# Optimization experiments

Hardware: AMD Instinct MI355X
Metric: run time of the kernel (lower is better)

The kernel has to match this reference:

```python
import jax, jax.numpy as jnp
import numpy as np
import math

NX = 240
XL = 6.0
A_ORB = 2
V0 = -20.0
S_INT = 0.5
ITERMAX = 500
FFAC = 0.4


def _wfho(n, x):
    # harmonic-oscillator eigenfunction (numpy, setup only)
    nfac = math.factorial(n)
    norm = (2.0 ** n * nfac) ** (-0.5) / math.pi ** 0.25
    if n == 0:
        Hn = np.ones_like(x)
    elif n == 1:
        Hn = 2.0 * x
    else:
        hm2 = np.ones_like(x)
        hm1 = 2.0 * x
        for m in range(2, n + 1):
            hmx = 2.0 * x * hm1 - 2.0 * (m - 1) * hm2
            hm2, hm1 = hm1, hmx
        Hn = hmx
    return norm * np.exp(-x ** 2 / 2.0) * Hn


def setup_inputs() -> dict:
    delx = 2.0 * XL / NX
    xx = delx * (np.arange(NX) - NX / 2.0)
    delp = 2.0 * math.pi / (2.0 * XL)
    pp = delp * (np.arange(NX) - NX / 2.0)
    # cder2[i,j] = sum_k exp(1j*(xj-xi)*pp_k) * pp_k^2 ; only real part is used
    D = xx[None, :] - xx[:, None]                      # [Nx, Nx], xj - xi
    cder2_re = np.cos(D[:, :, None] * pp[None, None, :]) @ (pp ** 2)
    der2 = -cder2_re * delx * delp / (2.0 * math.pi)
    kin = -der2 / 2.0
    pfac = 1.0 / abs(kin.max())
    U_HO = xx ** 2 / 2.0
    x1, x2 = np.meshgrid(xx, xx, indexing='ij')
    Vint = V0 * (2.0 * math.pi) ** (-0.5) / S_INT * np.exp(-(x1 - x2) ** 2 / (2.0 * S_INT ** 2))
    wfy0 = np.stack([_wfho(n, xx) for n in range(A_ORB)], axis=1)  # [Nx, Nmax]
    return {
        'wfy0': jnp.asarray(wfy0, jnp.float32),
        'kin_mat': jnp.asarray(kin, jnp.float32),
        'Vint': jnp.asarray(Vint, jnp.float32),
        'U_HO': jnp.asarray(U_HO, jnp.float32),
        'delx': jnp.float32(delx),
        'pfac': jnp.float32(pfac),
        'itermax': ITERMAX,
    }


def reference(wfy0, kin_mat, Vint, U_HO, delx, pfac, itermax):
    Nmax = wfy0.shape[1]
    delx = jnp.asarray(delx, jnp.float32).reshape(())
    pfac = jnp.asarray(pfac, jnp.float32).reshape(())

    def step(wfy, _):
        # densities from current orbitals
        hf_den = jnp.sum(wfy ** 2, axis=1)            # [Nx]
        hf_den_mat = wfy @ wfy.T                      # [Nx, Nx]
        Udir = delx * (Vint @ hf_den)
        Umf_mat = -delx * Vint * hf_den_mat
        Umf_mat = Umf_mat + jnp.diag(Udir + U_HO)     # add to diagonal
        H = kin_mat + Umf_mat

        updated = []
        spe = []
        ekin = jnp.float32(0.0)
        epot = jnp.float32(0.0)
        for ieig in range(Nmax):                      # Nmax=2, unrolled
            wf0 = wfy[:, ieig]
            wff = H @ wf0
            spe.append((wf0 @ wff) * delx)
            wfb = wf0 - wff * pfac
            norm = jnp.sum(wfb ** 2) * delx
            wff = wfb / jnp.sqrt(norm)
            for jeig in range(ieig):                  # Gram-Schmidt vs already-updated orbitals
                wff = wff - updated[jeig] * (updated[jeig] @ wff) * delx
            norm = jnp.sum(wff ** 2) * delx
            wff = wff / norm                          # faithful: divide by norm (not sqrt)
            new = FFAC * wff + (1.0 - FFAC) * wf0
            updated.append(new)
            ekin = ekin + (new @ (kin_mat @ new)) * delx
            epot = epot + (new @ (Umf_mat @ new)) * delx
        wfy_new = jnp.stack(updated, axis=1)

        esum0hf = spe[0]
        for s_ in spe[1:]:
            esum0hf = esum0hf + s_
        eho = jnp.sum(hf_den * U_HO) * delx / 2.0
        enerhfp = (esum0hf + ekin) / 2.0 + eho
        epot0hf = epot - 2.0 * eho
        enerhf = esum0hf - epot0hf / 2.0
        out = jnp.stack([enerhf, enerhfp, ekin, eho, epot0hf, esum0hf])
        return wfy_new, out

    _, outs = jax.lax.scan(step, wfy0, None, length=int(itermax))
    return outs[-1]  # (enerhf, enerhfp, ekin0hf, eho, epot0hf, esum0hf)
```

## Files before the change

kernel.cpp:

```cpp
#include <hip/hip_runtime.h>


#define NXX  240
#define NPAD 256
#define NTH  512
#define JCH  60
#define NBLK 15
#define NQW  16

template <int CTRL, int N>
__device__ __forceinline__ void dppStepN(float (&v)[N]) {
#pragma unroll
  for (int k = 0; k < N; ++k) {
    int s = __builtin_amdgcn_update_dpp(0, __float_as_int(v[k]), CTRL, 0xF, 0xF, false);
    v[k] += __int_as_float(s);
  }
}
template <int N>
__device__ __forceinline__ void waveSumDppN(float (&v)[N]) {
  dppStepN<0xB1>(v);
  dppStepN<0x4E>(v);
  dppStepN<0x141>(v);
  dppStepN<0x140>(v);
  dppStepN<0x142>(v);
  dppStepN<0x143>(v);
#pragma unroll
  for (int k = 0; k < N; ++k)
    v[k] = __int_as_float(__builtin_amdgcn_readlane(__float_as_int(v[k]), 63));
}

struct __align__(16) Smem {
  float cK[512];
  float cV[512];
  float uho[NPAD];
  float wfb[2][2][NPAD];
  float p00[NPAD];
  float p01[NPAD];
  float p11[NPAD];
  float part[4][6][NPAD];
};

__global__ void __launch_bounds__(NTH, 2)
hf_kernel(const float* __restrict__ wfy0,
          const float* __restrict__ kin,
          const float* __restrict__ vnt,
          const float* __restrict__ uho_g,
          const float* __restrict__ delx_p,
          const float* __restrict__ pfac_p,
          const int*   __restrict__ iter_p,
          float* __restrict__ out)
{
  __shared__ Smem sm;
  const int t  = (int)threadIdx.x;
  const int wv = t >> 6;
  const int l  = t & 63;
  const int i0 = 4 * l;
  const bool isK = (wv < 4);
  const int g  = isK ? wv : wv - 4;
  const int jg = g * JCH;
  const float delx = delx_p[0];
  const float pfac = pfac_p[0];
  const int itermax = iter_p[0];

  for (int a = t; a < 512; a += NTH) {
    int d = a - 256;
    float vk = 0.f, vv = 0.f;
    if (d >= 0 && d < NXX)      { vk = kin[(size_t)d * NXX]; vv = vnt[(size_t)d * NXX]; }
    else if (d < 0 && -d < NXX) { vk = kin[-d];              vv = vnt[-d]; }
    sm.cK[a] = vk; sm.cV[a] = vv;
  }
  if (t < NPAD) {
    float u  = (t < NXX) ? uho_g[t]        : 0.f;
    float a0 = (t < NXX) ? wfy0[2 * t]     : 0.f;
    float a1 = (t < NXX) ? wfy0[2 * t + 1] : 0.f;
    sm.uho[t] = u;
    sm.wfb[0][0][t] = a0; sm.wfb[0][1][t] = a1;
    sm.wfb[1][0][t] = 0.f; sm.wfb[1][1][t] = 0.f;
    sm.p00[t] = a0 * a0; sm.p01[t] = a0 * a1; sm.p11[t] = a1 * a1;
  }
  __syncthreads();

  const int qb = l - 15 * g + 49;
  const float* tab = isK ? sm.cK : sm.cV;
  float4 cw[NQW];
#pragma unroll
  for (int m = 0; m < NQW; ++m)
    cw[m] = *(const float4*)&tab[4 * (qb + m)];

  int cur = 0;
  for (int it = 0; it < itermax; ++it) {
    const bool last = (it == itermax - 1);
    const float* wf0 = sm.wfb[cur][0];
    const float* wf1 = sm.wfb[cur][1];
    float* nw0 = sm.wfb[cur ^ 1][0];
    float* nw1 = sm.wfb[cur ^ 1][1];

    if (isK) {
      float aK0[4] = {0,0,0,0}, aK1[4] = {0,0,0,0};
#pragma unroll
      for (int b = 0; b < NBLK; ++b) {
        const int j0 = jg + 4 * b;
        const float4 x0 = *(const float4*)&wf0[j0];
        const float4 x1 = *(const float4*)&wf1[j0];
        const float4 kh = cw[15 - b], kl = cw[14 - b];
        const float ck[8] = {kl.x, kl.y, kl.z, kl.w, kh.x, kh.y, kh.z, kh.w};
        const float xs0[4] = {x0.x, x0.y, x0.z, x0.w};
        const float xs1[4] = {x1.x, x1.y, x1.z, x1.w};
#pragma unroll
        for (int s = 0; s < 4; ++s) {
#pragma unroll
          for (int r = 0; r < 4; ++r) {
            const int c = 4 + r - s;
            aK0[r] = fmaf(xs0[s], ck[c], aK0[r]);
            aK1[r] = fmaf(xs1[s], ck[c], aK1[r]);
          }
        }
      }
      *(float4*)&sm.part[g][0][i0] = make_float4(aK0[0], aK0[1], aK0[2], aK0[3]);
      *(float4*)&sm.part[g][1][i0] = make_float4(aK1[0], aK1[1], aK1[2], aK1[3]);
    } else {
      float aV0[4] = {0,0,0,0}, aV1[4] = {0,0,0,0}, aV2[4] = {0,0,0,0};
#pragma unroll
      for (int b = 0; b < NBLK; ++b) {
        const int j0 = jg + 4 * b;
        const float4 y0 = *(const float4*)&sm.p00[j0];
        const float4 y1 = *(const float4*)&sm.p01[j0];
        const float4 y2 = *(const float4*)&sm.p11[j0];
        const float4 vh = cw[15 - b], vl = cw[14 - b];
        const float cv[8] = {vl.x, vl.y, vl.z, vl.w, vh.x, vh.y, vh.z, vh.w};
        const float ys0[4] = {y0.x, y0.y, y0.z, y0.w};
        const float ys1[4] = {y1.x, y1.y, y1.z, y1.w};
        const float ys2[4] = {y2.x, y2.y, y2.z, y2.w};
#pragma unroll
        for (int s = 0; s < 4; ++s) {
#pragma unroll
          for (int r = 0; r < 4; ++r) {
            const int c = 4 + r - s;
            aV0[r] = fmaf(ys0[s], cv[c], aV0[r]);
            aV1[r] = fmaf(ys1[s], cv[c], aV1[r]);
            aV2[r] = fmaf(ys2[s], cv[c], aV2[r]);
          }
        }
      }
      *(float4*)&sm.part[g][2][i0] = make_float4(aV0[0], aV0[1], aV0[2], aV0[3]);
      *(float4*)&sm.part[g][3][i0] = make_float4(aV1[0], aV1[1], aV1[2], aV1[3]);
      *(float4*)&sm.part[g][4][i0] = make_float4(aV2[0], aV2[1], aV2[2], aV2[3]);
    }
    __syncthreads();

    float w0[4], w1[4], Ut[4], wff0[4], wff1[4], new0[4], new1[4];
    float spe0 = 0.f, spe1 = 0.f, eho = 0.f;

    if (wv == 0) {
      const bool valid = (l < 60);
      float k0[4]  = {0,0,0,0}, k1[4]  = {0,0,0,0};
      float v00[4] = {0,0,0,0}, v01[4] = {0,0,0,0}, v11[4] = {0,0,0,0};
#pragma unroll
      for (int gg = 0; gg < 4; ++gg) {
        const float4 A0 = *(const float4*)&sm.part[gg][0][i0];
        const float4 A1 = *(const float4*)&sm.part[gg][1][i0];
        const float4 A2 = *(const float4*)&sm.part[gg][2][i0];
        const float4 A3 = *(const float4*)&sm.part[gg][3][i0];
        const float4 A4 = *(const float4*)&sm.part[gg][4][i0];
        k0[0]  += A0.x; k0[1]  += A0.y; k0[2]  += A0.z; k0[3]  += A0.w;
        k1[0]  += A1.x; k1[1]  += A1.y; k1[2]  += A1.z; k1[3]  += A1.w;
        v00[0] += A2.x; v00[1] += A2.y; v00[2] += A2.z; v00[3] += A2.w;
        v01[0] += A3.x; v01[1] += A3.y; v01[2] += A3.z; v01[3] += A3.w;
        v11[0] += A4.x; v11[1] += A4.y; v11[2] += A4.z; v11[3] += A4.w;
      }
      const float4 w0q = *(const float4*)&wf0[i0];
      const float4 w1q = *(const float4*)&wf1[i0];
      const float4 uq  = *(const float4*)&sm.uho[i0];
      w0[0] = w0q.x; w0[1] = w0q.y; w0[2] = w0q.z; w0[3] = w0q.w;
      w1[0] = w1q.x; w1[1] = w1q.y; w1[2] = w1q.z; w1[3] = w1q.w;
      const float uh[4] = {uq.x, uq.y, uq.z, uq.w};

      float wb0[4], wb1[4];
      float red[6] = {0, 0, 0, 0, 0, 0};
#pragma unroll
      for (int r = 0; r < 4; ++r) {
        Ut[r]   = delx * (v00[r] + v11[r]) + uh[r];
        wff0[r] = k0[r] - delx * (w0[r] * v00[r] + w1[r] * v01[r]) + Ut[r] * w0[r];
        wff1[r] = k1[r] - delx * (w0[r] * v01[r] + w1[r] * v11[r]) + Ut[r] * w1[r];
        wb0[r]  = w0[r] - pfac * wff0[r];
        wb1[r]  = w1[r] - pfac * wff1[r];
        if (!valid) { wb0[r] = 0.f; wb1[r] = 0.f; }
        red[0] += wb0[r] * wb0[r];
        red[1] += wb1[r] * wb1[r];
        red[2] += wb0[r] * wb1[r];
        red[3] += w0[r]  * wb1[r];
        red[4] += wb0[r] * w0[r];
        red[5] += w0[r]  * w0[r];
      }
      waveSumDppN<6>(red);
      const float rdelx = 1.f / delx;
      const float inv0 = 1.f / sqrtf(red[0] * delx);
      const float inv1 = 1.f / sqrtf(red[1] * delx);
      const float dB = delx * inv1 * (0.4f * red[2] * inv0 + 0.6f * red[3]);
      const float e0 = 0.16f * rdelx + 0.48f * red[4] * inv0 + 0.36f * red[5];
      const float sB = rdelx - dB * dB * (2.f * rdelx - e0);
      const float invB = 1.f / (sB * delx);
#pragma unroll
      for (int r = 0; r < 4; ++r) {
        const float wfA  = wb0[r] * inv0;
        const float wfBp = wb1[r] * inv1;
        new0[r] = 0.4f * wfA + 0.6f * w0[r];
        const float wfB2 = wfBp - new0[r] * dB;
        new1[r] = 0.4f * wfB2 * invB + 0.6f * w1[r];
      }
      *(float4*)&nw0[i0] = make_float4(new0[0], new0[1], new0[2], new0[3]);
      *(float4*)&nw1[i0] = make_float4(new1[0], new1[1], new1[2], new1[3]);
      *(float4*)&sm.p00[i0] =
          make_float4(new0[0]*new0[0], new0[1]*new0[1], new0[2]*new0[2], new0[3]*new0[3]);
      *(float4*)&sm.p01[i0] =
          make_float4(new0[0]*new1[0], new0[1]*new1[1], new0[2]*new1[2], new0[3]*new1[3]);
      *(float4*)&sm.p11[i0] =
          make_float4(new1[0]*new1[0], new1[1]*new1[1], new1[2]*new1[2], new1[3]*new1[3]);

      if (last) {
        float er[3] = {0, 0, 0};
#pragma unroll
        for (int r = 0; r < 4; ++r) {
          er[0] += w0[r] * wff0[r];
          er[1] += w1[r] * wff1[r];
          er[2] += (w0[r] * w0[r] + w1[r] * w1[r]) * uh[r];
        }
        waveSumDppN<3>(er);
        spe0 = er[0] * delx; spe1 = er[1] * delx; eho = er[2] * delx * 0.5f;
      }
    }
    __syncthreads();

    if (last) {
      if (isK) {
        float bA0[4] = {0,0,0,0}, bA1[4] = {0,0,0,0};
#pragma unroll
        for (int b = 0; b < NBLK; ++b) {
          const int j0 = jg + 4 * b;
          const float4 n0q = *(const float4*)&nw0[j0];
          const float4 n1q = *(const float4*)&nw1[j0];
          const float4 kh = cw[15 - b], kl = cw[14 - b];
          const float ck[8] = {kl.x, kl.y, kl.z, kl.w, kh.x, kh.y, kh.z, kh.w};
          const float xn0[4] = {n0q.x, n0q.y, n0q.z, n0q.w};
          const float xn1[4] = {n1q.x, n1q.y, n1q.z, n1q.w};
#pragma unroll
          for (int s = 0; s < 4; ++s) {
#pragma unroll
            for (int r = 0; r < 4; ++r) {
              const int c = 4 + r - s;
              bA0[r] = fmaf(xn0[s], ck[c], bA0[r]);
              bA1[r] = fmaf(xn1[s], ck[c], bA1[r]);
            }
          }
        }
        *(float4*)&sm.part[g][0][i0] = make_float4(bA0[0], bA0[1], bA0[2], bA0[3]);
        *(float4*)&sm.part[g][1][i0] = make_float4(bA1[0], bA1[1], bA1[2], bA1[3]);
      } else {
        float bV[4][4] = {};
#pragma unroll
        for (int b = 0; b < NBLK; ++b) {
          const int j0 = jg + 4 * b;
          const float4 o0q = *(const float4*)&wf0[j0];
          const float4 o1q = *(const float4*)&wf1[j0];
          const float4 n0q = *(const float4*)&nw0[j0];
          const float4 n1q = *(const float4*)&nw1[j0];
          const float4 vh = cw[15 - b], vl = cw[14 - b];
          const float cv[8] = {vl.x, vl.y, vl.z, vl.w, vh.x, vh.y, vh.z, vh.w};
          const float xo0[4] = {o0q.x, o0q.y, o0q.z, o0q.w};
          const float xo1[4] = {o1q.x, o1q.y, o1q.z, o1q.w};
          const float xn0[4] = {n0q.x, n0q.y, n0q.z, n0q.w};
          const float xn1[4] = {n1q.x, n1q.y, n1q.z, n1q.w};
#pragma unroll
          for (int s = 0; s < 4; ++s) {
            const float pr00 = xo0[s] * xn0[s];
            const float pr10 = xo1[s] * xn0[s];
            const float pr01 = xo0[s] * xn1[s];
            const float pr11 = xo1[s] * xn1[s];
#pragma unroll
            for (int r = 0; r < 4; ++r) {
              const int c = 4 + r - s;
              bV[0][r] = fmaf(pr00, cv[c], bV[0][r]);
              bV[1][r] = fmaf(pr10, cv[c], bV[1][r]);
              bV[2][r] = fmaf(pr01, cv[c], bV[2][r]);
              bV[3][r] = fmaf(pr11, cv[c], bV[3][r]);
            }
          }
        }
#pragma unroll
        for (int c2 = 0; c2 < 4; ++c2)
          *(float4*)&sm.part[g][2 + c2][i0] =
              make_float4(bV[c2][0], bV[c2][1], bV[c2][2], bV[c2][3]);
      }
      __syncthreads();

      if (wv == 0) {
        float rd[6][4] = {};
#pragma unroll
        for (int gg = 0; gg < 4; ++gg) {
#pragma unroll
          for (int c = 0; c < 6; ++c) {
            const float4 A = *(const float4*)&sm.part[gg][c][i0];
            rd[c][0] += A.x; rd[c][1] += A.y; rd[c][2] += A.z; rd[c][3] += A.w;
          }
        }
        float er[2] = {0, 0};
#pragma unroll
        for (int r = 0; r < 4; ++r) {
          const float um0 = -delx * (w0[r] * rd[2][r] + w1[r] * rd[3][r]) + Ut[r] * new0[r];
          const float um1 = -delx * (w0[r] * rd[4][r] + w1[r] * rd[5][r]) + Ut[r] * new1[r];
          er[0] += new0[r] * rd[0][r] + new1[r] * rd[1][r];
          er[1] += new0[r] * um0 + new1[r] * um1;
        }
        waveSumDppN<2>(er);
        const float ekin = er[0] * delx, epot = er[1] * delx;
        if (l == 0) {
          const float esum    = spe0 + spe1;
          const float enerhfp = 0.5f * (esum + ekin) + eho;
          const float epot0hf = epot - 2.f * eho;
          const float enerhf  = esum - 0.5f * epot0hf;
          out[0] = enerhf; out[1] = enerhfp; out[2] = ekin;
          out[3] = eho;    out[4] = epot0hf; out[5] = esum;
        }
      }
    }
    cur ^= 1;
  }
}

extern "C" void kernel_launch(void* const* d_in, const int* in_sizes, int n_in,
                              void* d_out, int out_size, void* d_ws, size_t ws_size,
                              hipStream_t stream) {
  const float* wfy0 = (const float*)d_in[0];
  const float* kin  = (const float*)d_in[1];
  const float* vnt  = (const float*)d_in[2];
  const float* uho  = (const float*)d_in[3];
  const float* delx = (const float*)d_in[4];
  const float* pfac = (const float*)d_in[5];
  const int*   itm  = (const int*)d_in[6];
  hipLaunchKernelGGL(hf_kernel, dim3(1), dim3(NTH), 0, stream,
                     wfy0, kin, vnt, uho, delx, pfac, itm, (float*)d_out);
}
```

Before: 1.282 ms.

## Use packed fp16 dot2 for Vint convolution and rebalance column chunks

The Vint (direct/exchange potential) convolution now stores the Toeplitz coefficients and the density products as packed fp16 pairs and accumulates with v_dot2_f32_f16, which halves the instruction count and LDS traffic for the V waves. Column chunks change from four equal 60-wide chunks to 64/64/64/48, which suits the packed layout. The V coefficients are now held per lane in a 66-entry register array. The cost is fp16 rounding of the interaction matrix and the densities, which may affect accuracy over 500 iterations, plus higher register pressure.

```diff
diff --git a/kernel.cpp b/kernel.cpp
--- a/kernel.cpp
+++ b/kernel.cpp
@@ -4,9 +4,24 @@
 #define NXX  240
 #define NPAD 256
 #define NTH  512
-#define JCH  60
-#define NBLK 15
-#define NQW  16
+
+typedef _Float16 h2 __attribute__((ext_vector_type(2)));
+
+__device__ __forceinline__ h2 bch2(unsigned u) { union { unsigned u; h2 h; } c; c.u = u; return c.h; }
+__device__ __forceinline__ unsigned bcu(h2 h)  { union { unsigned u; h2 h; } c; c.h = h; return c.u; }
+__device__ __forceinline__ unsigned pkh(float a, float b) {
+  h2 p; p.x = (_Float16)a; p.y = (_Float16)b; return bcu(p);
+}
+
+__device__ __forceinline__ float fdot2(h2 a, h2 b, float c) {
+#if __has_builtin(__builtin_amdgcn_fdot2)
+  return __builtin_amdgcn_fdot2(a, b, c, false);
+#else
+  float d;
+  asm("v_dot2_f32_f16 %0, %1, %2, %3" : "=v"(d) : "v"(a), "v"(b), "v"(c));
+  return d;
+#endif
+}
 
 template <int CTRL, int N>
 __device__ __forceinline__ void dppStepN(float (&v)[N]) {
@@ -31,14 +46,90 @@
 
 struct __align__(16) Smem {
   float cK[512];
-  float cV[512];
+  unsigned pkV[512];
   float uho[NPAD];
   float wfb[2][2][NPAD];
-  float p00[NPAD];
-  float p01[NPAD];
-  float p11[NPAD];
+  unsigned xpk[3][NPAD/2];
+  unsigned xprk[4][NPAD/2];
   float part[4][6][NPAD];
 };
+
+template <int NB>
+__device__ __forceinline__ void kinConv(const float* x0p, const float* x1p, int jg,
+                                        const float4* cw, float (&a0)[4], float (&a1)[4]) {
+#pragma unroll
+  for (int b = 0; b < NB; ++b) {
+    const int j0 = jg + 4 * b;
+    const float4 x0 = *(const float4*)&x0p[j0];
+    const float4 x1 = *(const float4*)&x1p[j0];
+    const float4 kh = cw[16 - b], kl = cw[15 - b];
+    const float ck[8] = {kl.x, kl.y, kl.z, kl.w, kh.x, kh.y, kh.z, kh.w};
+    const float xs0[4] = {x0.x, x0.y, x0.z, x0.w};
+    const float xs1[4] = {x1.x, x1.y, x1.z, x1.w};
+#pragma unroll
+    for (int s = 0; s < 4; ++s)
+#pragma unroll
+      for (int r = 0; r < 4; ++r) {
+        const int c = 4 + r - s;
+        a0[r] = fmaf(xs0[s], ck[c], a0[r]);
+        a1[r] = fmaf(xs1[s], ck[c], a1[r]);
+      }
+  }
+}
+
+template <int NSB>
+__device__ __forceinline__ void vConv3(const unsigned* q0, const unsigned* q1,
+                                       const unsigned* q2, int jg,
+                                       const unsigned* pkw, float (&A)[3][4]) {
+#pragma unroll
+  for (int sb = 0; sb < NSB; ++sb) {
+    const int base = jg / 2 + 4 * sb;
+    const uint4 X0 = *(const uint4*)&q0[base];
+    const uint4 X1 = *(const uint4*)&q1[base];
+    const uint4 X2 = *(const uint4*)&q2[base];
+    const unsigned xs0[4] = {X0.x, X0.y, X0.z, X0.w};
+    const unsigned xs1[4] = {X1.x, X1.y, X1.z, X1.w};
+    const unsigned xs2[4] = {X2.x, X2.y, X2.z, X2.w};
+#pragma unroll
+    for (int p = 0; p < 4; ++p)
+#pragma unroll
+      for (int r = 0; r < 4; ++r) {
+        const int tt = r - 2 * p - 8 * sb + (NSB * 8 - 2);
+        const h2 c = bch2(pkw[tt]);
+        A[0][r] = fdot2(c, bch2(xs0[p]), A[0][r]);
+        A[1][r] = fdot2(c, bch2(xs1[p]), A[1][r]);
+        A[2][r] = fdot2(c, bch2(xs2[p]), A[2][r]);
+      }
+  }
+}
+
+template <int NSB>
+__device__ __forceinline__ void vConv4(const unsigned (*q)[NPAD / 2], int jg,
+                                       const unsigned* pkw, float (&A)[4][4]) {
+#pragma unroll
+  for (int sb = 0; sb < NSB; ++sb) {
+    const int base = jg / 2 + 4 * sb;
+    const uint4 X0 = *(const uint4*)&q[0][base];
+    const uint4 X1 = *(const uint4*)&q[1][base];
+    const uint4 X2 = *(const uint4*)&q[2][base];
+    const uint4 X3 = *(const uint4*)&q[3][base];
+    const unsigned xs0[4] = {X0.x, X0.y, X0.z, X0.w};
+    const unsigned xs1[4] = {X1.x, X1.y, X1.z, X1.w};
+    const unsigned xs2[4] = {X2.x, X2.y, X2.z, X2.w};
+    const unsigned xs3[4] = {X3.x, X3.y, X3.z, X3.w};
+#pragma unroll
+    for (int p = 0; p < 4; ++p)
+#pragma unroll
+      for (int r = 0; r < 4; ++r) {
+        const int tt = r - 2 * p - 8 * sb + (NSB * 8 - 2);
+        const h2 c = bch2(pkw[tt]);
+        A[0][r] = fdot2(c, bch2(xs0[p]), A[0][r]);
+        A[1][r] = fdot2(c, bch2(xs1[p]), A[1][r]);
+        A[2][r] = fdot2(c, bch2(xs2[p]), A[2][r]);
+        A[3][r] = fdot2(c, bch2(xs3[p]), A[3][r]);
+      }
+  }
+}
 
 __global__ void __launch_bounds__(NTH, 2)
 hf_kernel(const float* __restrict__ wfy0,
@@ -57,17 +148,25 @@
   const int i0 = 4 * l;
   const bool isK = (wv < 4);
   const int g  = isK ? wv : wv - 4;
-  const int jg = g * JCH;
+  const int jg = 64 * g;
+  const int len = (g < 3) ? 64 : 48;
   const float delx = delx_p[0];
   const float pfac = pfac_p[0];
   const int itermax = iter_p[0];
 
   for (int a = t; a < 512; a += NTH) {
     int d = a - 256;
-    float vk = 0.f, vv = 0.f;
-    if (d >= 0 && d < NXX)      { vk = kin[(size_t)d * NXX]; vv = vnt[(size_t)d * NXX]; }
-    else if (d < 0 && -d < NXX) { vk = kin[-d];              vv = vnt[-d]; }
-    sm.cK[a] = vk; sm.cV[a] = vv;
+    float vk = 0.f;
+    if (d >= 0 && d < NXX)      vk = kin[(size_t)d * NXX];
+    else if (d < 0 && -d < NXX) vk = kin[-d];
+    sm.cK[a] = vk;
+    float vh = 0.f, vl = 0.f;
+    if (d >= 0 && d < NXX)      vh = vnt[(size_t)d * NXX];
+    else if (d < 0 && -d < NXX) vh = vnt[-d];
+    int d2 = d - 1;
+    if (d2 >= 0 && d2 < NXX)      vl = vnt[(size_t)d2 * NXX];
+    else if (d2 < 0 && -d2 < NXX) vl = vnt[-d2];
+    sm.pkV[a] = pkh(vh, vl);
   }
   if (t < NPAD) {
     float u  = (t < NXX) ? uho_g[t]        : 0.f;
@@ -76,16 +175,31 @@
     sm.uho[t] = u;
     sm.wfb[0][0][t] = a0; sm.wfb[0][1][t] = a1;
     sm.wfb[1][0][t] = 0.f; sm.wfb[1][1][t] = 0.f;
-    sm.p00[t] = a0 * a0; sm.p01[t] = a0 * a1; sm.p11[t] = a1 * a1;
+  }
+  if (t < NPAD / 2) {
+    int j0 = 2 * t, j1 = 2 * t + 1;
+    float w00 = (j0 < NXX) ? wfy0[2 * j0]     : 0.f;
+    float w01 = (j0 < NXX) ? wfy0[2 * j0 + 1] : 0.f;
+    float w10 = (j1 < NXX) ? wfy0[2 * j1]     : 0.f;
+    float w11 = (j1 < NXX) ? wfy0[2 * j1 + 1] : 0.f;
+    sm.xpk[0][t] = pkh(w00 * w00, w10 * w10);
+    sm.xpk[1][t] = pkh(w00 * w01, w10 * w11);
+    sm.xpk[2][t] = pkh(w01 * w01, w11 * w11);
   }
   __syncthreads();
 
-  const int qb = l - 15 * g + 49;
-  const float* tab = isK ? sm.cK : sm.cV;
-  float4 cw[NQW];
-#pragma unroll
-  for (int m = 0; m < NQW; ++m)
-    cw[m] = *(const float4*)&tab[4 * (qb + m)];
+  float4 cw[17];
+  if (isK) {
+    const int qbase = l - 16 * g + 48;
+#pragma unroll
+    for (int m = 0; m < 17; ++m) cw[m] = *(const float4*)&sm.cK[4 * (qbase + m)];
+  }
+  unsigned pkw[66];
+  if (!isK) {
+    const int Abase = i0 - jg - (len - 2) + 256;
+#pragma unroll
+    for (int m = 0; m < 66; ++m) pkw[m] = sm.pkV[Abase + m];
+  }
 
   int cur = 0;
   for (int it = 0; it < itermax; ++it) {
@@ -96,55 +210,19 @@
     float* nw1 = sm.wfb[cur ^ 1][1];
 
     if (isK) {
-      float aK0[4] = {0,0,0,0}, aK1[4] = {0,0,0,0};
-#pragma unroll
-      for (int b = 0; b < NBLK; ++b) {
-        const int j0 = jg + 4 * b;
-        const float4 x0 = *(const float4*)&wf0[j0];
-        const float4 x1 = *(const float4*)&wf1[j0];
-        const float4 kh = cw[15 - b], kl = cw[14 - b];
-        const float ck[8] = {kl.x, kl.y, kl.z, kl.w, kh.x, kh.y, kh.z, kh.w};
-        const float xs0[4] = {x0.x, x0.y, x0.z, x0.w};
-        const float xs1[4] = {x1.x, x1.y, x1.z, x1.w};
-#pragma unroll
-        for (int s = 0; s < 4; ++s) {
-#pragma unroll
-          for (int r = 0; r < 4; ++r) {
-            const int c = 4 + r - s;
-            aK0[r] = fmaf(xs0[s], ck[c], aK0[r]);
-            aK1[r] = fmaf(xs1[s], ck[c], aK1[r]);
-          }
-        }
-      }
+      float aK0[4] = {0, 0, 0, 0}, aK1[4] = {0, 0, 0, 0};
+      if (g < 3) kinConv<16>(wf0, wf1, jg, cw, aK0, aK1);
+      else       kinConv<12>(wf0, wf1, jg, cw, aK0, aK1);
       *(float4*)&sm.part[g][0][i0] = make_float4(aK0[0], aK0[1], aK0[2], aK0[3]);
       *(float4*)&sm.part[g][1][i0] = make_float4(aK1[0], aK1[1], aK1[2], aK1[3]);
     } else {
-      float aV0[4] = {0,0,0,0}, aV1[4] = {0,0,0,0}, aV2[4] = {0,0,0,0};
-#pragma unroll
-      for (int b = 0; b < NBLK; ++b) {
-        const int j0 = jg + 4 * b;
-        const float4 y0 = *(const float4*)&sm.p00[j0];
-        const float4 y1 = *(const float4*)&sm.p01[j0];
-        const float4 y2 = *(const float4*)&sm.p11[j0];
-        const float4 vh = cw[15 - b], vl = cw[14 - b];
-        const float cv[8] = {vl.x, vl.y, vl.z, vl.w, vh.x, vh.y, vh.z, vh.w};
-        const float ys0[4] = {y0.x, y0.y, y0.z, y0.w};
-        const float ys1[4] = {y1.x, y1.y, y1.z, y1.w};
-        const float ys2[4] = {y2.x, y2.y, y2.z, y2.w};
-#pragma unroll
-        for (int s = 0; s < 4; ++s) {
-#pragma unroll
-          for (int r = 0; r < 4; ++r) {
-            const int c = 4 + r - s;
-            aV0[r] = fmaf(ys0[s], cv[c], aV0[r]);
-            aV1[r] = fmaf(ys1[s], cv[c], aV1[r]);
-            aV2[r] = fmaf(ys2[s], cv[c], aV2[r]);
-          }
-        }
-      }
-      *(float4*)&sm.part[g][2][i0] = make_float4(aV0[0], aV0[1], aV0[2], aV0[3]);
-      *(float4*)&sm.part[g][3][i0] = make_float4(aV1[0], aV1[1], aV1[2], aV1[3]);
-      *(float4*)&sm.part[g][4][i0] = make_float4(aV2[0], aV2[1], aV2[2], aV2[3]);
+      float aV[3][4] = {};
+      if (g < 3) vConv3<8>(sm.xpk[0], sm.xpk[1], sm.xpk[2], jg, pkw, aV);
+      else       vConv3<6>(sm.xpk[0], sm.xpk[1], sm.xpk[2], jg, pkw, aV);
+#pragma unroll
+      for (int c = 0; c < 3; ++c)
+        *(float4*)&sm.part[g][2 + c][i0] =
+            make_float4(aV[c][0], aV[c][1], aV[c][2], aV[c][3]);
     }
     __syncthreads();
 
@@ -153,8 +231,8 @@
 
     if (wv == 0) {
       const bool valid = (l < 60);
-      float k0[4]  = {0,0,0,0}, k1[4]  = {0,0,0,0};
-      float v00[4] = {0,0,0,0}, v01[4] = {0,0,0,0}, v11[4] = {0,0,0,0};
+      float k0[4]  = {0, 0, 0, 0}, k1[4]  = {0, 0, 0, 0};
+      float v00[4] = {0, 0, 0, 0}, v01[4] = {0, 0, 0, 0}, v11[4] = {0, 0, 0, 0};
 #pragma unroll
       for (int gg = 0; gg < 4; ++gg) {
         const float4 A0 = *(const float4*)&sm.part[gg][0][i0];
@@ -210,12 +288,15 @@
       }
       *(float4*)&nw0[i0] = make_float4(new0[0], new0[1], new0[2], new0[3]);
       *(float4*)&nw1[i0] = make_float4(new1[0], new1[1], new1[2], new1[3]);
-      *(float4*)&sm.p00[i0] =
-          make_float4(new0[0]*new0[0], new0[1]*new0[1], new0[2]*new0[2], new0[3]*new0[3]);
-      *(float4*)&sm.p01[i0] =
-          make_float4(new0[0]*new1[0], new0[1]*new1[1], new0[2]*new1[2], new0[3]*new1[3]);
-      *(float4*)&sm.p11[i0] =
-          make_float4(new1[0]*new1[0], new1[1]*new1[1], new1[2]*new1[2], new1[3]*new1[3]);
+      *(uint2*)&sm.xpk[0][2 * l] = make_uint2(
+          pkh(new0[0] * new0[0], new0[1] * new0[1]),
+          pkh(new0[2] * new0[2], new0[3] * new0[3]));
+      *(uint2*)&sm.xpk[1][2 * l] = make_uint2(
+          pkh(new0[0] * new1[0], new0[1] * new1[1]),
+          pkh(new0[2] * new1[2], new0[3] * new1[3]));
+      *(uint2*)&sm.xpk[2][2 * l] = make_uint2(
+          pkh(new1[0] * new1[0], new1[1] * new1[1]),
+          pkh(new1[2] * new1[2], new1[3] * new1[3]));
 
       if (last) {
         float er[3] = {0, 0, 0};
@@ -232,60 +313,28 @@
     __syncthreads();
 
     if (last) {
+      if (t < NPAD / 2) {
+        const float2 o0 = *(const float2*)&wf0[2 * t];
+        const float2 o1 = *(const float2*)&wf1[2 * t];
+        const float2 n0 = *(const float2*)&nw0[2 * t];
+        const float2 n1 = *(const float2*)&nw1[2 * t];
+        sm.xprk[0][t] = pkh(o0.x * n0.x, o0.y * n0.y);
+        sm.xprk[1][t] = pkh(o1.x * n0.x, o1.y * n0.y);
+        sm.xprk[2][t] = pkh(o0.x * n1.x, o0.y * n1.y);
+        sm.xprk[3][t] = pkh(o1.x * n1.x, o1.y * n1.y);
+      }
+      __syncthreads();
+
       if (isK) {
-        float bA0[4] = {0,0,0,0}, bA1[4] = {0,0,0,0};
-#pragma unroll
-        for (int b = 0; b < NBLK; ++b) {
-          const int j0 = jg + 4 * b;
-          const float4 n0q = *(const float4*)&nw0[j0];
-          const float4 n1q = *(const float4*)&nw1[j0];
-          const float4 kh = cw[15 - b], kl = cw[14 - b];
-          const float ck[8] = {kl.x, kl.y, kl.z, kl.w, kh.x, kh.y, kh.z, kh.w};
-          const float xn0[4] = {n0q.x, n0q.y, n0q.z, n0q.w};
-          const float xn1[4] = {n1q.x, n1q.y, n1q.z, n1q.w};
-#pragma unroll
-          for (int s = 0; s < 4; ++s) {
-#pragma unroll
-            for (int r = 0; r < 4; ++r) {
-              const int c = 4 + r - s;
-              bA0[r] = fmaf(xn0[s], ck[c], bA0[r]);
-              bA1[r] = fmaf(xn1[s], ck[c], bA1[r]);
-            }
-          }
-        }
+        float bA0[4] = {0, 0, 0, 0}, bA1[4] = {0, 0, 0, 0};
+        if (g < 3) kinConv<16>(nw0, nw1, jg, cw, bA0, bA1);
+        else       kinConv<12>(nw0, nw1, jg, cw, bA0, bA1);
         *(float4*)&sm.part[g][0][i0] = make_float4(bA0[0], bA0[1], bA0[2], bA0[3]);
         *(float4*)&sm.part[g][1][i0] = make_float4(bA1[0], bA1[1], bA1[2], bA1[3]);
       } else {
         float bV[4][4] = {};
-#pragma unroll
-        for (int b = 0; b < NBLK; ++b) {
-          const int j0 = jg + 4 * b;
-          const float4 o0q = *(const float4*)&wf0[j0];
-          const float4 o1q = *(const float4*)&wf1[j0];
-          const float4 n0q = *(const float4*)&nw0[j0];
-          const float4 n1q = *(const float4*)&nw1[j0];
-          const float4 vh = cw[15 - b], vl = cw[14 - b];
-          const float cv[8] = {vl.x, vl.y, vl.z, vl.w, vh.x, vh.y, vh.z, vh.w};
-          const float xo0[4] = {o0q.x, o0q.y, o0q.z, o0q.w};
-          const float xo1[4] = {o1q.x, o1q.y, o1q.z, o1q.w};
-          const float xn0[4] = {n0q.x, n0q.y, n0q.z, n0q.w};
-          const float xn1[4] = {n1q.x, n1q.y, n1q.z, n1q.w};
-#pragma unroll
-          for (int s = 0; s < 4; ++s) {
-            const float pr00 = xo0[s] * xn0[s];
-            const float pr10 = xo1[s] * xn0[s];
-            const float pr01 = xo0[s] * xn1[s];
-            const float pr11 = xo1[s] * xn1[s];
-#pragma unroll
-            for (int r = 0; r < 4; ++r) {
-              const int c = 4 + r - s;
-              bV[0][r] = fmaf(pr00, cv[c], bV[0][r]);
-              bV[1][r] = fmaf(pr10, cv[c], bV[1][r]);
-              bV[2][r] = fmaf(pr01, cv[c], bV[2][r]);
-              bV[3][r] = fmaf(pr11, cv[c], bV[3][r]);
-            }
-          }
-        }
+        if (g < 3) vConv4<8>(sm.xprk, jg, pkw, bV);
+        else       vConv4<6>(sm.xprk, jg, pkw, bV);
 #pragma unroll
         for (int c2 = 0; c2 < 4; ++c2)
           *(float4*)&sm.part[g][2 + c2][i0] =
@@ -296,13 +345,12 @@
       if (wv == 0) {
         float rd[6][4] = {};
 #pragma unroll
-        for (int gg = 0; gg < 4; ++gg) {
+        for (int gg = 0; gg < 4; ++gg)
 #pragma unroll
           for (int c = 0; c < 6; ++c) {
             const float4 A = *(const float4*)&sm.part[gg][c][i0];
             rd[c][0] += A.x; rd[c][1] += A.y; rd[c][2] += A.z; rd[c][3] += A.w;
           }
-        }
         float er[2] = {0, 0};
 #pragma unroll
         for (int r = 0; r < 4; ++r) {
```

Measured after the change: 3.142 ms. 2.45x slower.
